# Performance work log

Hardware: AMD Instinct MI355X
Metric: run time of the kernel (lower is better)

Reference implementation:

```python
import jax, jax.numpy as jnp
import numpy as np

N_CHANNEL = 64
N_BAND = 5
N_CLASS = 2
B = 64
K = 2 * N_CHANNEL  # nodes covered by the fully-connected edge_index


def _w(key, shape):
    fan_in = shape[0] if len(shape) == 2 else int(np.prod(shape[1:]))
    return (jax.random.normal(key, shape, jnp.float32) / np.float32(np.sqrt(fan_in)))


def setup_inputs() -> dict:
    key = jax.random.key(0)
    ks = jax.random.split(key, 22)
    d = {}
    d['x1'] = jax.random.normal(ks[0], (B, K, N_BAND), jnp.float32)
    d['x2'] = jax.random.normal(ks[1], (B, K, K), jnp.float32)
    # GCNConv params (weights stored (in, out); PyG applies linear then aggregates, bias after)
    d['gcn1_w'] = _w(ks[2], (N_BAND, 2 * N_BAND))
    d['gcn1_b'] = 0.01 * jax.random.normal(ks[3], (2 * N_BAND,), jnp.float32)
    d['gcn2_w'] = _w(ks[4], (2 * N_BAND, 1))
    d['gcn2_b'] = 0.01 * jax.random.normal(ks[5], (1,), jnp.float32)
    d['fcg_w'] = _w(ks[6], (K, K))
    d['fcg_b'] = 0.01 * jax.random.normal(ks[7], (K,), jnp.float32)
    d['conv1_w'] = _w(ks[8], (16, 1, 3, 3))   # OIHW
    d['conv1_b'] = 0.01 * jax.random.normal(ks[9], (16,), jnp.float32)
    d['conv2_w'] = _w(ks[10], (16, 16, 3, 3))
    d['conv2_b'] = 0.01 * jax.random.normal(ks[11], (16,), jnp.float32)
    d['fcc_w'] = _w(ks[12], (16 * K * K, K))
    d['fcc_b'] = 0.01 * jax.random.normal(ks[13], (K,), jnp.float32)
    d['fc1_w'] = _w(ks[14], (4 * N_CHANNEL, 2 * N_CHANNEL))
    d['fc1_b'] = 0.01 * jax.random.normal(ks[15], (2 * N_CHANNEL,), jnp.float32)
    d['fc2_w'] = _w(ks[16], (2 * N_CHANNEL, N_CHANNEL))
    d['fc2_b'] = 0.01 * jax.random.normal(ks[17], (N_CHANNEL,), jnp.float32)
    d['fc3_w'] = _w(ks[18], (N_CHANNEL, N_CLASS))
    d['fc3_b'] = 0.01 * jax.random.normal(ks[19], (N_CLASS,), jnp.float32)
    return d


def _gcn(x, W, b):
    # Faithful to original: edge_index is fully connected over the FIRST K rows only.
    # With default self-loops, normalized adjacency over rows [0,K) is (1/K)*ones(K,K)
    # (all degrees = K); every other row has only its self-loop (degree 1 -> identity).
    y = x @ W                                   # (B*N, out)
    y = y.at[:K].set(jnp.mean(y[:K], axis=0))   # broadcast mean over first K rows
    return y + b


def _conv(x, w, b):
    y = jax.lax.conv_general_dilated(x, w, (1, 1), 'SAME',
                                     dimension_numbers=('NCHW', 'OIHW', 'NCHW'))
    return jax.nn.relu(y + b[None, :, None, None])


def reference(x1, x2, gcn1_w, gcn1_b, gcn2_w, gcn2_b, fcg_w, fcg_b,
              conv1_w, conv1_b, conv2_w, conv2_b, fcc_w, fcc_b,
              fc1_w, fc1_b, fc2_w, fc2_b, fc3_w, fc3_b):
    Bn, N, Feat = x1.shape
    # GNN branch (dropout is identity in eval mode)
    h = x1.reshape(Bn * N, Feat)
    h = jax.nn.relu(_gcn(h, gcn1_w, gcn1_b))
    h = jax.nn.relu(_gcn(h, gcn2_w, gcn2_b))
    h = h.reshape(Bn, -1)                       # (B, 2*n_channel)
    g = jax.nn.relu(h @ fcg_w + fcg_b)
    # CNN branch
    c = x2[:, None]                             # (B,1,H,W)
    c = _conv(c, conv1_w, conv1_b)
    c = _conv(c, conv2_w, conv2_b)
    c = c.reshape(Bn, -1)                       # channel-major flatten, same as torch .view
    c = jax.nn.relu(c @ fcc_w + fcc_b)
    # Fusion MLP
    x = jnp.concatenate([c, g], axis=1)
    x = jax.nn.relu(x @ fc1_w + fc1_b)
    x = jax.nn.relu(x @ fc2_w + fc2_b)
    return jax.nn.sigmoid(x @ fc3_w + fc3_b)
```

## Files before the change

kernel.cpp:

```cpp
#include <hip/hip_runtime.h>
#include <hip/hip_bf16.h>


#define NROWS   8192
#define IMG     16384
#define FCC_K   262144
#define FCC_BLOCKS 512
#define FCC_KRANGE 512
#define FCC_CHUNK 128
#define WPAD 132

typedef __attribute__((ext_vector_type(8))) short bf16x8;
typedef __attribute__((ext_vector_type(4))) float f32x4;
typedef __attribute__((ext_vector_type(4))) unsigned short us4;
typedef __attribute__((ext_vector_type(8))) unsigned short us8;

__device__ __forceinline__ unsigned short f2bf(float f) {
    unsigned u = __float_as_uint(f);
    unsigned r = (u + 0x7FFFu + ((u >> 16) & 1u)) >> 16;
    return (unsigned short)r;
}

__global__ __launch_bounds__(128) void gcnfcg_kernel(
    const float* __restrict__ x1,
    const float* __restrict__ W1,
    const float* __restrict__ b1,
    const float* __restrict__ W2,
    const float* __restrict__ b2,
    const float* __restrict__ fcgW,
    const float* __restrict__ fcgb,
    float* __restrict__ g)
{
    __shared__ float sW1[50], sb1[10], sW2[10], smean[10];
    __shared__ float sy1[128][10];
    __shared__ float sh2[128];
    int b = blockIdx.x, t = threadIdx.x;
    if (t < 50) sW1[t] = W1[t];
    if (t < 10) { sb1[t] = b1[t]; sW2[t] = W2[t]; }
    __syncthreads();

    int r = b*128 + t;
    float x[5];
    #pragma unroll
    for (int f = 0; f < 5; ++f) x[f] = x1[r*5 + f];
    float y[10];
    #pragma unroll
    for (int o = 0; o < 10; ++o) {
        float a = 0.f;
        #pragma unroll
        for (int f = 0; f < 5; ++f) a += x[f] * sW1[f*10 + o];
        y[o] = a;
    }

    float h1row[10];
    if (b == 0) {
        #pragma unroll
        for (int o = 0; o < 10; ++o) sy1[t][o] = y[o];
        __syncthreads();
        if (t < 10) {
            float s = 0.f;
            for (int rr = 0; rr < 128; ++rr) s += sy1[rr][t];
            smean[t] = fmaxf(s * (1.f/128.f) + sb1[t], 0.f);
        }
        __syncthreads();
        #pragma unroll
        for (int o = 0; o < 10; ++o) h1row[o] = smean[o];
    } else {
        #pragma unroll
        for (int o = 0; o < 10; ++o) h1row[o] = fmaxf(y[o] + sb1[o], 0.f);
    }

    float y2 = 0.f;
    #pragma unroll
    for (int o = 0; o < 10; ++o) y2 += h1row[o] * sW2[o];
    sh2[t] = fmaxf(y2 + b2[0], 0.f);
    __syncthreads();

    float acc = fcgb[t];
    #pragma unroll 8
    for (int k = 0; k < 128; ++k) acc += sh2[k] * fcgW[k*128 + t];
    g[b*128 + t] = fmaxf(acc, 0.f);
}

__global__ __launch_bounds__(256) void conv12_kernel(
    const float* __restrict__ x2,
    const float* __restrict__ w1,
    const float* __restrict__ b1,
    const float* __restrict__ w2,
    const float* __restrict__ b2,
    unsigned short* __restrict__ c2bf)
{
    __shared__ float sx2[8][130];
    __shared__ unsigned short sin[6*130*16];
    __shared__ unsigned short sB[5*512];
    __shared__ float sw1[144], sb1v[16];

    int tid = threadIdx.x;
    int blk = blockIdx.x;
    int b   = blk >> 5;
    int R0  = (blk & 31) * 4;

    if (tid < 144) sw1[tid] = w1[tid];
    if (tid < 16)  sb1v[tid] = b1[tid];

    for (int idx = tid; idx < 2560; idx += 256) {
        int q   = idx >> 9;
        int rem = idx & 511;
        int l   = rem >> 3;
        int e   = rem & 7;
        int k   = (l >> 4) * 8 + e;
        int oc  = l & 15;
        int ic  = k & 15;
        int dd  = 2*q + (k >> 4);
        unsigned short bits = 0;
        if (dd < 9) bits = f2bf(w2[oc*144 + ic*9 + dd]);
        sB[idx] = bits;
    }
    if (tid < 192) {
        int rr = tid >> 5, rem = tid & 31;
        int cc = (rem < 16) ? 0 : 129;
        sin[(rr*130 + cc)*16 + (rem & 15)] = 0;
    }
    {
        const float* xb = x2 + (size_t)b * IMG;
        for (int idx = tid; idx < 8*130; idx += 256) {
            int rr = idx / 130, cc = idx - rr*130;
            int ri = R0 - 2 + rr, gj = cc - 1;
            float v = 0.f;
            if (ri >= 0 && ri < 128 && gj >= 0 && gj < 128)
                v = xb[ri*128 + gj];
            sx2[rr][cc] = v;
        }
    }
    __syncthreads();

    for (int p = tid; p < 768; p += 256) {
        int rr = p >> 7;
        int cc = p & 127;
        int ri1 = R0 - 1 + rr;
        bool valid = (ri1 >= 0 && ri1 < 128);
        float in9[3][3];
        #pragma unroll
        for (int di = 0; di < 3; ++di)
          #pragma unroll
          for (int dj = 0; dj < 3; ++dj)
              in9[di][dj] = sx2[rr + di][cc + dj];
        us8 o0, o1;
        #pragma unroll
        for (int oc = 0; oc < 16; ++oc) {
            float acc = sb1v[oc];
            #pragma unroll
            for (int di = 0; di < 3; ++di)
              #pragma unroll
              for (int dj = 0; dj < 3; ++dj)
                  acc += in9[di][dj] * sw1[oc*9 + di*3 + dj];
            unsigned short bits = valid ? f2bf(fmaxf(acc, 0.f)) : (unsigned short)0;
            if (oc < 8) o0[oc] = bits; else o1[oc - 8] = bits;
        }
        unsigned short* dst = &sin[(rr*130 + cc + 1)*16];
        *reinterpret_cast<us8*>(dst)     = o0;
        *reinterpret_cast<us8*>(dst + 8) = o1;
    }
    __syncthreads();

    int lane = tid & 63;
    int wv   = tid >> 6;
    int ln   = lane & 15;
    int g    = lane >> 4;
    int ghalf = g & 1;

    int aoff[5];
    #pragma unroll
    for (int q = 0; q < 5; ++q) {
        int dd = 2*q + (g >> 1);
        if (dd > 8) dd = 8;
        int di = dd / 3, dj = dd % 3;
        aoff[q] = ((wv + di)*130 + ln + dj)*16 + ghalf*8;
    }

    bf16x8 bf[5];
    #pragma unroll
    for (int q = 0; q < 5; ++q)
        bf[q] = *reinterpret_cast<const bf16x8*>(&sB[q*512 + lane*8]);

    float bias_oc = b2[ln];
    int r = R0 + wv;
    unsigned short* outbase = c2bf + ((size_t)b*16 + ln)*IMG + r*128;

    #pragma unroll
    for (int t = 0; t < 8; ++t) {
        f32x4 acc = {0.f, 0.f, 0.f, 0.f};
        #pragma unroll
        for (int q = 0; q < 5; ++q) {
            bf16x8 a = *reinterpret_cast<const bf16x8*>(&sin[aoff[q] + t*256]);
            acc = __builtin_amdgcn_mfma_f32_16x16x32_bf16(a, bf[q], acc, 0, 0, 0);
        }
        int pc = t*16 + g*4;
        #pragma unroll
        for (int reg = 0; reg < 4; ++reg)
            outbase[pc + reg] = f2bf(fmaxf(acc[reg] + bias_oc, 0.f));
    }
}

__global__ __launch_bounds__(256, 4) void fcc_mfma(
    const unsigned short* __restrict__ c2bf,
    const float* __restrict__ W,
    float* __restrict__ partials)
{
    __shared__ unsigned short sW[FCC_CHUNK * WPAD];

    int tid  = threadIdx.x;
    int blk  = blockIdx.x;
    int k0   = blk * FCC_KRANGE;
    int lane = tid & 63, wv = tid >> 6;
    int ln   = lane & 15, g = lane >> 4;

    f32x4 acc[8];
    #pragma unroll
    for (int j = 0; j < 8; ++j) acc[j] = (f32x4){0.f,0.f,0.f,0.f};

    int skr = tid >> 5;
    int sn0 = (tid & 31) * 4;

    for (int kc = 0; kc < FCC_KRANGE; kc += FCC_CHUNK) {
        #pragma unroll 4
        for (int it = 0; it < 16; ++it) {
            int k = skr + it*8;
            float4 v = *reinterpret_cast<const float4*>(
                W + (size_t)(k0 + kc + k)*128 + sn0);
            us4 pk;
            pk[0] = f2bf(v.x); pk[1] = f2bf(v.y);
            pk[2] = f2bf(v.z); pk[3] = f2bf(v.w);
            *reinterpret_cast<us4*>(&sW[k*WPAD + sn0]) = pk;
        }
        __syncthreads();

        #pragma unroll
        for (int ks = 0; ks < 4; ++ks) {
            const unsigned short* ap = c2bf + (size_t)(16*wv + ln)*FCC_K
                                       + k0 + kc + ks*32 + g*8;
            bf16x8 afrag = *reinterpret_cast<const bf16x8*>(ap);
            int rbase = (ks*32 + g*8) * WPAD;
            #pragma unroll
            for (int j = 0; j < 8; ++j) {
                int col = j*16 + ln;
                bf16x8 bfrag;
                #pragma unroll
                for (int e = 0; e < 8; ++e)
                    bfrag[e] = (short)sW[rbase + e*WPAD + col];
                acc[j] = __builtin_amdgcn_mfma_f32_16x16x32_bf16(afrag, bfrag, acc[j], 0, 0, 0);
            }
        }
        __syncthreads();
    }

    float* p = partials + (size_t)blk * 8192;
    #pragma unroll
    for (int j = 0; j < 8; ++j)
      #pragma unroll
      for (int reg = 0; reg < 4; ++reg) {
          int m = 16*wv + g*4 + reg;
          p[m*128 + j*16 + ln] = acc[j][reg];
      }
}

__global__ __launch_bounds__(256) void fcc_reduce(
    const float* __restrict__ partials,
    const float* __restrict__ bias,
    float* __restrict__ cvec)
{
    __shared__ float sred[4][64];
    int blk = blockIdx.x;
    int t = threadIdx.x;
    int o = blk*64 + (t & 63);
    int pr = t >> 6;
    float s = 0.f;
    #pragma unroll 4
    for (int p = pr; p < FCC_BLOCKS; p += 4)
        s += partials[(size_t)p*8192 + o];
    sred[pr][t & 63] = s;
    __syncthreads();
    if (t < 64) {
        float v = sred[0][t] + sred[1][t] + sred[2][t] + sred[3][t];
        cvec[o] = fmaxf(v + bias[o & 127], 0.f);
    }
}

__global__ __launch_bounds__(128) void head_kernel(
    const float* __restrict__ cvec, const float* __restrict__ g,
    const float* __restrict__ w1, const float* __restrict__ bb1,
    const float* __restrict__ w2, const float* __restrict__ bb2,
    const float* __restrict__ w3, const float* __restrict__ bb3,
    float* __restrict__ out)
{
    __shared__ float sx[256], sh[128], s2[64];
    int b = blockIdx.x, tid = threadIdx.x;
    sx[tid]       = cvec[b*128 + tid];
    sx[128 + tid] = g[b*128 + tid];
    __syncthreads();
    {
        float acc = bb1[tid];
        for (int k = 0; k < 256; ++k) acc += sx[k] * w1[k*128 + tid];
        sh[tid] = fmaxf(acc, 0.f);
    }
    __syncthreads();
    if (tid < 64) {
        float acc = bb2[tid];
        for (int k = 0; k < 128; ++k) acc += sh[k] * w2[k*64 + tid];
        s2[tid] = fmaxf(acc, 0.f);
    }
    __syncthreads();
    if (tid < 2) {
        float acc = bb3[tid];
        for (int k = 0; k < 64; ++k) acc += s2[k] * w3[k*2 + tid];
        out[b*2 + tid] = 1.f / (1.f + __expf(-acc));
    }
}

extern "C" void kernel_launch(void* const* d_in, const int* in_sizes, int n_in,
                              void* d_out, int out_size, void* d_ws, size_t ws_size,
                              hipStream_t stream)
{
    const float* x1      = (const float*)d_in[0];
    const float* x2      = (const float*)d_in[1];
    const float* gcn1_w  = (const float*)d_in[2];
    const float* gcn1_b  = (const float*)d_in[3];
    const float* gcn2_w  = (const float*)d_in[4];
    const float* gcn2_b  = (const float*)d_in[5];
    const float* fcg_w   = (const float*)d_in[6];
    const float* fcg_b   = (const float*)d_in[7];
    const float* conv1_w = (const float*)d_in[8];
    const float* conv1_b = (const float*)d_in[9];
    const float* conv2_w = (const float*)d_in[10];
    const float* conv2_b = (const float*)d_in[11];
    const float* fcc_w   = (const float*)d_in[12];
    const float* fcc_b   = (const float*)d_in[13];
    const float* fc1_w   = (const float*)d_in[14];
    const float* fc1_b   = (const float*)d_in[15];
    const float* fc2_w   = (const float*)d_in[16];
    const float* fc2_b   = (const float*)d_in[17];
    const float* fc3_w   = (const float*)d_in[18];
    const float* fc3_b   = (const float*)d_in[19];
    float* out = (float*)d_out;

    float* ws = (float*)d_ws;
    float* g        = ws;
    unsigned short* c2bf = (unsigned short*)(g + 8192);
    float* partials = (float*)(c2bf + 16777216);
    float* cvec     = partials + 4194304;

    gcnfcg_kernel<<<64, 128, 0, stream>>>(x1, gcn1_w, gcn1_b, gcn2_w, gcn2_b,
                                          fcg_w, fcg_b, g);
    conv12_kernel<<<2048, 256, 0, stream>>>(x2, conv1_w, conv1_b,
                                            conv2_w, conv2_b, c2bf);
    fcc_mfma<<<FCC_BLOCKS, 256, 0, stream>>>(c2bf, fcc_w, partials);
    fcc_reduce<<<128, 256, 0, stream>>>(partials, fcc_b, cvec);
    head_kernel<<<64, 128, 0, stream>>>(cvec, g, fc1_w, fc1_b, fc2_w, fc2_b,
                                        fc3_w, fc3_b, out);
}
```

Before: 100.6 us.

## Prefetch FCC weights into registers, pre-swizzle LDS fragments, fuse reduce into head

The FCC MFMA kernel now prefetches the next weight chunk into registers while the current chunk is computed. It stores bf16 weights in LDS already packed in fragment order, with a lane rotation to avoid bank conflicts, so each B fragment is a single 16-byte LDS load instead of eight scalar loads. The separate partial-sum reduction kernel is removed and folded into the head kernel, saving one launch. The cost is more registers (launch bounds lowered to 3 waves) and a head kernel where each thread serially sums 512 partials, which may be slower than the old parallel reduce.

```diff
diff --git a/kernel.cpp b/kernel.cpp
--- a/kernel.cpp
+++ b/kernel.cpp
@@ -8,7 +8,6 @@
 #define FCC_BLOCKS 512
 #define FCC_KRANGE 512
 #define FCC_CHUNK 128
-#define WPAD 132
 
 typedef __attribute__((ext_vector_type(8))) short bf16x8;
 typedef __attribute__((ext_vector_type(4))) float f32x4;
@@ -202,12 +201,12 @@
     }
 }
 
-__global__ __launch_bounds__(256, 4) void fcc_mfma(
+__global__ __launch_bounds__(256, 3) void fcc_mfma(
     const unsigned short* __restrict__ c2bf,
     const float* __restrict__ W,
     float* __restrict__ partials)
 {
-    __shared__ unsigned short sW[FCC_CHUNK * WPAD];
+    __shared__ unsigned short sWp[4*8*64*8];
 
     int tid  = threadIdx.x;
     int blk  = blockIdx.x;
@@ -219,39 +218,75 @@
     #pragma unroll
     for (int j = 0; j < 8; ++j) acc[j] = (f32x4){0.f,0.f,0.f,0.f};
 
-    int skr = tid >> 5;
-    int sn0 = (tid & 31) * 4;
-
-    for (int kc = 0; kc < FCC_KRANGE; kc += FCC_CHUNK) {
-        #pragma unroll 4
-        for (int it = 0; it < 16; ++it) {
-            int k = skr + it*8;
-            float4 v = *reinterpret_cast<const float4*>(
-                W + (size_t)(k0 + kc + k)*128 + sn0);
-            us4 pk;
-            pk[0] = f2bf(v.x); pk[1] = f2bf(v.y);
-            pk[2] = f2bf(v.z); pk[3] = f2bf(v.w);
-            *reinterpret_cast<us4*>(&sW[k*WPAD + sn0]) = pk;
-        }
-        __syncthreads();
-
+    const float* Wb = W + (size_t)k0 * 128;
+    const unsigned short* arow = c2bf + (size_t)(16*wv + ln)*FCC_K + k0 + g*8;
+
+    float4 vbuf[16];
+
+    #pragma unroll
+    for (int it = 0; it < 16; ++it) {
+        int f = it*256 + tid;
+        vbuf[it] = *reinterpret_cast<const float4*>(Wb + (size_t)(f >> 5)*128 + (f & 31)*4);
+    }
+    #pragma unroll
+    for (int it = 0; it < 16; ++it) {
+        int f = it*256 + tid;
+        int k = f >> 5, col4 = f & 31;
+        int kk = k & 31, ks = k >> 5, e = kk & 7, grp = kk >> 3;
+        float vv[4] = {vbuf[it].x, vbuf[it].y, vbuf[it].z, vbuf[it].w};
+        #pragma unroll
+        for (int c = 0; c < 4; ++c) {
+            int col = col4*4 + c;
+            int j   = col >> 4;
+            int l   = grp*16 + (col & 15);
+            int ls  = (l + j) & 63;
+            sWp[((ks*8 + j)*64 + ls)*8 + e] = f2bf(vv[c]);
+        }
+    }
+    __syncthreads();
+
+    #pragma unroll
+    for (int ci = 0; ci < 4; ++ci) {
+        if (ci < 3) {
+            const float* Wc = Wb + (size_t)(ci + 1) * FCC_CHUNK * 128;
+            #pragma unroll
+            for (int it = 0; it < 16; ++it) {
+                int f = it*256 + tid;
+                vbuf[it] = *reinterpret_cast<const float4*>(Wc + (size_t)(f >> 5)*128 + (f & 31)*4);
+            }
+        }
+        bf16x8 af[4];
+        #pragma unroll
+        for (int ks = 0; ks < 4; ++ks)
+            af[ks] = *reinterpret_cast<const bf16x8*>(arow + ci*FCC_CHUNK + ks*32);
         #pragma unroll
         for (int ks = 0; ks < 4; ++ks) {
-            const unsigned short* ap = c2bf + (size_t)(16*wv + ln)*FCC_K
-                                       + k0 + kc + ks*32 + g*8;
-            bf16x8 afrag = *reinterpret_cast<const bf16x8*>(ap);
-            int rbase = (ks*32 + g*8) * WPAD;
             #pragma unroll
             for (int j = 0; j < 8; ++j) {
-                int col = j*16 + ln;
-                bf16x8 bfrag;
+                bf16x8 bfrag = *reinterpret_cast<const bf16x8*>(
+                    &sWp[((ks*8 + j)*64 + ((lane + j) & 63))*8]);
+                acc[j] = __builtin_amdgcn_mfma_f32_16x16x32_bf16(af[ks], bfrag, acc[j], 0, 0, 0);
+            }
+        }
+        __syncthreads();
+        if (ci < 3) {
+            #pragma unroll
+            for (int it = 0; it < 16; ++it) {
+                int f = it*256 + tid;
+                int k = f >> 5, col4 = f & 31;
+                int kk = k & 31, ks = k >> 5, e = kk & 7, grp = kk >> 3;
+                float vv[4] = {vbuf[it].x, vbuf[it].y, vbuf[it].z, vbuf[it].w};
                 #pragma unroll
-                for (int e = 0; e < 8; ++e)
-                    bfrag[e] = (short)sW[rbase + e*WPAD + col];
-                acc[j] = __builtin_amdgcn_mfma_f32_16x16x32_bf16(afrag, bfrag, acc[j], 0, 0, 0);
+                for (int c = 0; c < 4; ++c) {
+                    int col = col4*4 + c;
+                    int j   = col >> 4;
+                    int l   = grp*16 + (col & 15);
+                    int ls  = (l + j) & 63;
+                    sWp[((ks*8 + j)*64 + ls)*8 + e] = f2bf(vv[c]);
+                }
             }
-        }
-        __syncthreads();
+            __syncthreads();
+        }
     }
 
     float* p = partials + (size_t)blk * 8192;
@@ -264,30 +299,10 @@
       }
 }
 
-__global__ __launch_bounds__(256) void fcc_reduce(
+__global__ __launch_bounds__(128) void head_kernel(
     const float* __restrict__ partials,
-    const float* __restrict__ bias,
-    float* __restrict__ cvec)
-{
-    __shared__ float sred[4][64];
-    int blk = blockIdx.x;
-    int t = threadIdx.x;
-    int o = blk*64 + (t & 63);
-    int pr = t >> 6;
-    float s = 0.f;
-    #pragma unroll 4
-    for (int p = pr; p < FCC_BLOCKS; p += 4)
-        s += partials[(size_t)p*8192 + o];
-    sred[pr][t & 63] = s;
-    __syncthreads();
-    if (t < 64) {
-        float v = sred[0][t] + sred[1][t] + sred[2][t] + sred[3][t];
-        cvec[o] = fmaxf(v + bias[o & 127], 0.f);
-    }
-}
-
-__global__ __launch_bounds__(128) void head_kernel(
-    const float* __restrict__ cvec, const float* __restrict__ g,
+    const float* __restrict__ fccb,
+    const float* __restrict__ g,
     const float* __restrict__ w1, const float* __restrict__ bb1,
     const float* __restrict__ w2, const float* __restrict__ bb2,
     const float* __restrict__ w3, const float* __restrict__ bb3,
@@ -295,7 +310,12 @@
 {
     __shared__ float sx[256], sh[128], s2[64];
     int b = blockIdx.x, tid = threadIdx.x;
-    sx[tid]       = cvec[b*128 + tid];
+
+    const float* pb = partials + (size_t)b*128 + tid;
+    float s = 0.f;
+    #pragma unroll 8
+    for (int p = 0; p < FCC_BLOCKS; ++p) s += pb[(size_t)p*8192];
+    sx[tid]       = fmaxf(s + fccb[tid], 0.f);
     sx[128 + tid] = g[b*128 + tid];
     __syncthreads();
     {
@@ -347,14 +367,12 @@
     float* g        = ws;
     unsigned short* c2bf = (unsigned short*)(g + 8192);
     float* partials = (float*)(c2bf + 16777216);
-    float* cvec     = partials + 4194304;
 
     gcnfcg_kernel<<<64, 128, 0, stream>>>(x1, gcn1_w, gcn1_b, gcn2_w, gcn2_b,
                                           fcg_w, fcg_b, g);
     conv12_kernel<<<2048, 256, 0, stream>>>(x2, conv1_w, conv1_b,
                                             conv2_w, conv2_b, c2bf);
     fcc_mfma<<<FCC_BLOCKS, 256, 0, stream>>>(c2bf, fcc_w, partials);
-    fcc_reduce<<<128, 256, 0, stream>>>(partials, fcc_b, cvec);
-    head_kernel<<<64, 128, 0, stream>>>(cvec, g, fc1_w, fc1_b, fc2_w, fc2_b,
-                                        fc3_w, fc3_b, out);
-}
+    head_kernel<<<64, 128, 0, stream>>>(partials, fcc_b, g, fc1_w, fc1_b,
+                                        fc2_w, fc2_b, fc3_w, fc3_b, out);
+}
```

After: 136.3 us. 35.5% more time.
